# Kernel optimization log

Measured on AMD Instinct MI355X. Metric: run time of the kernel, lower is better.

Reference implementation:

```python
import jax, jax.numpy as jnp
import numpy as np

N_BINS = 15

def setup_inputs() -> dict:
    key = jax.random.key(0)
    k1, k2 = jax.random.split(key)
    N, C = 1048576, 128
    logits = jax.random.normal(k1, (N, C), dtype=jnp.float32)
    labels = jax.random.randint(k2, (N,), 0, C, dtype=jnp.int64)
    return {"logits": logits, "labels": labels}

def reference(logits, labels):
    # softmax + argmax: confidences = max prob, predictions = argmax
    probs = jax.nn.softmax(logits, axis=1)
    conf = jnp.max(probs, axis=1)                      # [N]
    pred = jnp.argmax(probs, axis=1)                   # [N]
    acc = (pred == labels).astype(conf.dtype)          # [N]
    # bin i covers (i/n_bins, (i+1)/n_bins]; conf > 1/C > 0 so ceil-1 lands in-range
    bins = jnp.clip(jnp.ceil(conf * N_BINS).astype(jnp.int32) - 1, 0, N_BINS - 1)
    ones = jnp.ones_like(conf)
    counts = jax.ops.segment_sum(ones, bins, num_segments=N_BINS)
    conf_sum = jax.ops.segment_sum(conf, bins, num_segments=N_BINS)
    acc_sum = jax.ops.segment_sum(acc, bins, num_segments=N_BINS)
    n = jnp.asarray(conf.shape[0], conf.dtype)
    safe = jnp.maximum(counts, 1.0)
    per_bin = jnp.abs(conf_sum / safe - acc_sum / safe) * (counts / n)
    ece = jnp.sum(jnp.where(counts > 0, per_bin, 0.0))
    return ece.reshape(1)
```

## Files before the change

### kernel.cpp

```cpp
#include <hip/hip_runtime.h>

#define N_BINS 15
#define GRID_MAIN 2048
#define BLOCK 256
#define ROWS_PER_HW 4

__global__ __launch_bounds__(BLOCK) void ece_main(const float* __restrict__ logits,
                                                  const int* __restrict__ labels,
                                                  float* __restrict__ partial,
                                                  int N, int nBlocks) {
    __shared__ float s_acc[3 * N_BINS];
    const int tid = threadIdx.x;
    if (tid < 3 * N_BINS) s_acc[tid] = 0.f;
    __syncthreads();

    const int hw  = tid >> 5;
    const int sub = tid & 31;

    auto process = [&](const float4 v, int row) {
        float m = v.x; int mi = sub * 4;
        if (v.y > m) { m = v.y; mi = sub * 4 + 1; }
        if (v.z > m) { m = v.z; mi = sub * 4 + 2; }
        if (v.w > m) { m = v.w; mi = sub * 4 + 3; }
        #pragma unroll
        for (int off = 16; off > 0; off >>= 1) {
            float om = __shfl_xor(m, off);
            int   oi = __shfl_xor(mi, off);
            if (om > m || (om == m && oi < mi)) { m = om; mi = oi; }
        }
        float s = __expf(v.x - m) + __expf(v.y - m) + __expf(v.z - m) + __expf(v.w - m);
        #pragma unroll
        for (int off = 16; off > 0; off >>= 1)
            s += __shfl_xor(s, off);
        if (sub == 0) {
            const float conf = 1.0f / s;
            int bin = (int)ceilf(conf * (float)N_BINS) - 1;
            bin = min(max(bin, 0), N_BINS - 1);
            const float acc = (mi == labels[row]) ? 1.0f : 0.0f;
            atomicAdd(&s_acc[bin],              1.0f);
            atomicAdd(&s_acc[N_BINS + bin],     conf);
            atomicAdd(&s_acc[2 * N_BINS + bin], acc);
        }
    };

    const int rowsPerIter = (BLOCK >> 5) * ROWS_PER_HW;
    const int rowStride   = nBlocks * rowsPerIter;

    for (int base = blockIdx.x * rowsPerIter + hw * ROWS_PER_HW; base < N; base += rowStride) {
        float4 v[ROWS_PER_HW];
        bool   has[ROWS_PER_HW];
        #pragma unroll
        for (int j = 0; j < ROWS_PER_HW; ++j) {
            has[j] = (base + j) < N;
            if (has[j]) v[j] = ((const float4*)(logits + (size_t)(base + j) * 128))[sub];
        }
        #pragma unroll
        for (int j = 0; j < ROWS_PER_HW; ++j)
            if (has[j]) process(v[j], base + j);
    }

    __syncthreads();
    if (tid < 3 * N_BINS)
        partial[(size_t)tid * nBlocks + blockIdx.x] = s_acc[tid];
}

__global__ __launch_bounds__(1024) void ece_final(const float* __restrict__ partial,
                                                  float* __restrict__ out,
                                                  int nBlocks, float invN) {
    __shared__ float red[3 * N_BINS];
    const int tid = threadIdx.x;
    const int w = tid >> 6, lane = tid & 63;
    for (int s = w; s < 3 * N_BINS; s += 16) {
        float sum = 0.f;
        for (int i = lane; i < nBlocks; i += 64)
            sum += partial[(size_t)s * nBlocks + i];
        #pragma unroll
        for (int off = 32; off > 0; off >>= 1)
            sum += __shfl_xor(sum, off);
        if (lane == 0) red[s] = sum;
    }
    __syncthreads();
    if (tid == 0) {
        float ece = 0.f;
        #pragma unroll
        for (int b = 0; b < N_BINS; ++b) {
            if (red[b] > 0.f)
                ece += fabsf(red[N_BINS + b] - red[2 * N_BINS + b]) * invN;
        }
        out[0] = ece;
    }
}

extern "C" void kernel_launch(void* const* d_in, const int* in_sizes, int n_in,
                              void* d_out, int out_size, void* d_ws, size_t ws_size,
                              hipStream_t stream) {
    const float* logits = (const float*)d_in[0];
    const int*   labels = (const int*)d_in[1];
    float*       out    = (float*)d_out;
    float*       partial = (float*)d_ws;

    const int N = in_sizes[1];

    int grid = GRID_MAIN;
    const int rowsPerIter = (BLOCK >> 5) * ROWS_PER_HW;
    if ((size_t)grid * rowsPerIter > (size_t)N)
        grid = (N + rowsPerIter - 1) / rowsPerIter;

    ece_main<<<grid, BLOCK, 0, stream>>>(logits, labels, partial, N, grid);
    ece_final<<<1, 1024, 0, stream>>>(partial, out, grid, 1.0f / (float)N);
}
```

Baseline: 717.3 us.

## Use 16-lane row groups with two float4 loads and nontemporal streaming

Each row is now handled by 16 lanes that each load two float4 vectors, so a 256-thread block covers twice as many rows per iteration and the shuffle reductions drop from five steps to four. Full tiles use nontemporal loads for the logits and prefetch the labels ahead of the compute loop. A guarded tail path handles partial tiles. This aims to raise memory-level parallelism on a bandwidth-bound read of about 512 MB, at the cost of more registers per thread and a duplicated code path.

```diff
diff --git a/kernel.cpp b/kernel.cpp
--- a/kernel.cpp
+++ b/kernel.cpp
@@ -3,7 +3,9 @@
 #define N_BINS 15
 #define GRID_MAIN 2048
 #define BLOCK 256
-#define ROWS_PER_HW 4
+#define ROWS_PER_GRP 4
+
+typedef float f32x4 __attribute__((ext_vector_type(4)));
 
 __global__ __launch_bounds__(BLOCK) void ece_main(const float* __restrict__ logits,
                                                   const int* __restrict__ labels,
@@ -14,49 +16,68 @@
     if (tid < 3 * N_BINS) s_acc[tid] = 0.f;
     __syncthreads();
 
-    const int hw  = tid >> 5;
-    const int sub = tid & 31;
+    const int grp = tid >> 4;
+    const int sub = tid & 15;
 
-    auto process = [&](const float4 v, int row) {
-        float m = v.x; int mi = sub * 4;
-        if (v.y > m) { m = v.y; mi = sub * 4 + 1; }
-        if (v.z > m) { m = v.z; mi = sub * 4 + 2; }
-        if (v.w > m) { m = v.w; mi = sub * 4 + 3; }
+    auto process = [&](const f32x4 a, const f32x4 b, int lab, int row) {
+        const int i0 = sub * 4, i1 = 64 + sub * 4;
+        float m = a[0]; int mi = i0;
+        if (a[1] > m) { m = a[1]; mi = i0 + 1; }
+        if (a[2] > m) { m = a[2]; mi = i0 + 2; }
+        if (a[3] > m) { m = a[3]; mi = i0 + 3; }
+        if (b[0] > m) { m = b[0]; mi = i1; }
+        if (b[1] > m) { m = b[1]; mi = i1 + 1; }
+        if (b[2] > m) { m = b[2]; mi = i1 + 2; }
+        if (b[3] > m) { m = b[3]; mi = i1 + 3; }
         #pragma unroll
-        for (int off = 16; off > 0; off >>= 1) {
+        for (int off = 8; off > 0; off >>= 1) {
             float om = __shfl_xor(m, off);
             int   oi = __shfl_xor(mi, off);
             if (om > m || (om == m && oi < mi)) { m = om; mi = oi; }
         }
-        float s = __expf(v.x - m) + __expf(v.y - m) + __expf(v.z - m) + __expf(v.w - m);
+        float s = __expf(a[0] - m) + __expf(a[1] - m) + __expf(a[2] - m) + __expf(a[3] - m)
+                + __expf(b[0] - m) + __expf(b[1] - m) + __expf(b[2] - m) + __expf(b[3] - m);
         #pragma unroll
-        for (int off = 16; off > 0; off >>= 1)
+        for (int off = 8; off > 0; off >>= 1)
             s += __shfl_xor(s, off);
         if (sub == 0) {
             const float conf = 1.0f / s;
             int bin = (int)ceilf(conf * (float)N_BINS) - 1;
             bin = min(max(bin, 0), N_BINS - 1);
-            const float acc = (mi == labels[row]) ? 1.0f : 0.0f;
+            const float acc = (mi == lab) ? 1.0f : 0.0f;
             atomicAdd(&s_acc[bin],              1.0f);
             atomicAdd(&s_acc[N_BINS + bin],     conf);
             atomicAdd(&s_acc[2 * N_BINS + bin], acc);
         }
     };
 
-    const int rowsPerIter = (BLOCK >> 5) * ROWS_PER_HW;
+    const int rowsPerIter = (BLOCK >> 4) * ROWS_PER_GRP;
     const int rowStride   = nBlocks * rowsPerIter;
 
-    for (int base = blockIdx.x * rowsPerIter + hw * ROWS_PER_HW; base < N; base += rowStride) {
-        float4 v[ROWS_PER_HW];
-        bool   has[ROWS_PER_HW];
-        #pragma unroll
-        for (int j = 0; j < ROWS_PER_HW; ++j) {
-            has[j] = (base + j) < N;
-            if (has[j]) v[j] = ((const float4*)(logits + (size_t)(base + j) * 128))[sub];
+    for (int tile = blockIdx.x * rowsPerIter; tile < N; tile += rowStride) {
+        const int base = tile + grp * ROWS_PER_GRP;
+        if (tile + rowsPerIter <= N) {
+            f32x4 va[ROWS_PER_GRP], vb[ROWS_PER_GRP];
+            int   lab[ROWS_PER_GRP];
+            #pragma unroll
+            for (int j = 0; j < ROWS_PER_GRP; ++j) {
+                const f32x4* rp = (const f32x4*)(logits + (size_t)(base + j) * 128);
+                va[j]  = __builtin_nontemporal_load(rp + sub);
+                vb[j]  = __builtin_nontemporal_load(rp + 16 + sub);
+                lab[j] = labels[base + j];
+            }
+            #pragma unroll
+            for (int j = 0; j < ROWS_PER_GRP; ++j)
+                process(va[j], vb[j], lab[j], base + j);
+        } else {
+            #pragma unroll
+            for (int j = 0; j < ROWS_PER_GRP; ++j) {
+                if (base + j < N) {
+                    const f32x4* rp = (const f32x4*)(logits + (size_t)(base + j) * 128);
+                    process(rp[sub], rp[16 + sub], labels[base + j], base + j);
+                }
+            }
         }
-        #pragma unroll
-        for (int j = 0; j < ROWS_PER_HW; ++j)
-            if (has[j]) process(v[j], base + j);
     }
 
     __syncthreads();
@@ -102,7 +123,7 @@
     const int N = in_sizes[1];
 
     int grid = GRID_MAIN;
-    const int rowsPerIter = (BLOCK >> 5) * ROWS_PER_HW;
+    const int rowsPerIter = (BLOCK >> 4) * ROWS_PER_GRP;
     if ((size_t)grid * rowsPerIter > (size_t)N)
         grid = (N + rowsPerIter - 1) / rowsPerIter;
 
```

New measurement: 682.6 us. 1.05x faster.
